# Optimization experiments

Hardware: AMD Instinct MI355X
Metric: run time of the kernel (lower is better)

Reference implementation:

```python
import jax, jax.numpy as jnp
import numpy as np

NUM_HEADS = 16
HEAD_DIM = 128
RMS_EPS = 1e-6


def _rms_norm(x):
    # RMSNorm over last dim, no learned weight
    return x * jax.lax.rsqrt(jnp.mean(jnp.square(x), axis=-1, keepdims=True) + RMS_EPS)


def _rotary_cos_sin(T, head_dim, dtype=jnp.float32):
    # half-truncated RoPE: quarter of dims get frequencies, next quarter gets freq 0
    dim_quarter = max(1, head_dim // 4)
    angular_freq = (1.0 / 1024.0) ** jnp.linspace(0.0, 1.0, dim_quarter, dtype=dtype)
    angular_freq = jnp.concatenate([angular_freq, jnp.zeros(dim_quarter, dtype=dtype)])  # [head_dim//2]
    t = jnp.arange(T, dtype=dtype)
    theta = t[:, None] * angular_freq[None, :]  # [T, head_dim//2]
    return jnp.cos(theta), jnp.sin(theta)


def _apply_rotary(x_BTHD, cos, sin):
    # x: [B,T,H,D]; cos/sin: [T, D//2]
    c = cos[None, :, None, :]
    s = sin[None, :, None, :]
    x1, x2 = jnp.split(x_BTHD, 2, axis=-1)
    y1 = x1 * c + x2 * s
    y2 = -x1 * s + x2 * c
    return jnp.concatenate([y1, y2], axis=-1)


def setup_inputs() -> dict:
    key = jax.random.key(0)
    k1, k2, k3 = jax.random.split(key, 3)
    B, T, dim = 1, 2048, 2048
    hdim = NUM_HEADS * HEAD_DIM
    std = 0.5 * dim ** (-0.5)
    x = jax.random.normal(k1, (B, T, dim), dtype=jnp.float32)
    Wqkv = jax.random.normal(k2, (3, hdim, dim), dtype=jnp.float32) * std
    Wout = jax.random.normal(k3, (dim, hdim), dtype=jnp.float32) * std
    return {"x": x, "Wqkv": Wqkv, "Wout": Wout}


def reference(x, Wqkv, Wout):
    B, T, dim = x.shape
    H, D = NUM_HEADS, HEAD_DIM
    scale = 1.0 / (D ** 0.5)

    # fused QKV projection: [B,T,3,H,D]
    qkv = jnp.einsum('btd,ehd->bteh'.replace('eh', 'f'), x, Wqkv.reshape(3 * H * D, dim))  # [B,T,3HD]
    qkv = qkv.reshape(B, T, 3, H, D)
    q, k, v = qkv[:, :, 0], qkv[:, :, 1], qkv[:, :, 2]  # each [B,T,H,D]

    q, k = _rms_norm(q), _rms_norm(k)
    cos, sin = _rotary_cos_sin(T, D, dtype=jnp.float32)
    q, k = _apply_rotary(q, cos, sin), _apply_rotary(k, cos, sin)

    # causal attention
    scores = jnp.einsum('bthd,bshd->bhts', q, k) * scale  # [B,H,T,T]
    causal = jnp.tril(jnp.ones((T, T), dtype=bool))
    scores = jnp.where(causal[None, None], scores, -jnp.inf)
    probs = jax.nn.softmax(scores, axis=-1)
    y = jnp.einsum('bhts,bshd->bthd', probs, v)  # [B,T,H,D]

    y = y.reshape(B, T, H * D)
    return y @ Wout.T
```

## Files before the change

### kernel.cpp

```cpp
#include <hip/hip_runtime.h>
#include <hip/hip_bf16.h>
#include <stdint.h>

typedef __hip_bfloat16 bf16;
typedef __bf16 bf16x8 __attribute__((ext_vector_type(8)));
typedef float f32x4 __attribute__((ext_vector_type(4)));

#define MFMA16(a, b, c) __builtin_amdgcn_mfma_f32_16x16x32_bf16((a), (b), (c), 0, 0, 0)

__device__ __forceinline__ void gload_lds16(const void* g, void* l) {
    __builtin_amdgcn_global_load_lds((const __attribute__((address_space(1))) void*)g,
                                     (__attribute__((address_space(3))) void*)l, 16, 0, 0);
}

struct alignas(16) B8 { bf16 v[8]; };
struct alignas(8)  B4 { bf16 v[4]; };

__global__ __launch_bounds__(256) void cast_all_k(
    const float* __restrict__ x, const float* __restrict__ wqkv, const float* __restrict__ wout,
    bf16* __restrict__ xb, bf16* __restrict__ wqkvb, bf16* __restrict__ woutb) {
    const size_t NX = (size_t)2048 * 2048 / 8;
    const size_t NW = (size_t)3 * 2048 * 2048 / 8;
    size_t i = (size_t)blockIdx.x * 256 + threadIdx.x;
    const float* s; bf16* d;
    if (i < NX)            { s = x;    d = xb; }
    else if (i < NX + NW)  { s = wqkv; d = wqkvb; i -= NX; }
    else                   { s = wout; d = woutb; i -= NX + NW; }
    float4 a = ((const float4*)s)[2 * i];
    float4 b = ((const float4*)s)[2 * i + 1];
    B8 t;
    t.v[0] = __float2bfloat16(a.x); t.v[1] = __float2bfloat16(a.y);
    t.v[2] = __float2bfloat16(a.z); t.v[3] = __float2bfloat16(a.w);
    t.v[4] = __float2bfloat16(b.x); t.v[5] = __float2bfloat16(b.y);
    t.v[6] = __float2bfloat16(b.z); t.v[7] = __float2bfloat16(b.w);
    ((B8*)d)[i] = t;
}

__global__ __launch_bounds__(256) void gemm_bt(
    const bf16* __restrict__ A, const bf16* __restrict__ B, float* __restrict__ C,
    int M, int N, int K) {
    __shared__ __align__(16) bf16 As[128 * 32];
    __shared__ __align__(16) bf16 Bs[128 * 32];
    const int t = threadIdx.x;
    const int lane = t & 63, w = t >> 6;
    const int wr = w >> 1, wc = w & 1;
    const int l15 = lane & 15, lg = lane >> 4;
    const int m0 = blockIdx.y * 128, n0 = blockIdx.x * 128;

    f32x4 acc[4][4] = {};

    for (int k0 = 0; k0 < K; k0 += 32) {
#pragma unroll
        for (int c = 0; c < 2; ++c) {
            int f = t + c * 256;
            int row = f >> 2, cb = f & 3;
            gload_lds16(&A[(size_t)(m0 + row) * K + k0 + cb * 8], &As[f * 8]);
            gload_lds16(&B[(size_t)(n0 + row) * K + k0 + cb * 8], &Bs[f * 8]);
        }
        __syncthreads();

        bf16x8 af[4], bfr[4];
#pragma unroll
        for (int mi = 0; mi < 4; ++mi)
            af[mi] = *(const bf16x8*)&As[(wr * 64 + mi * 16 + l15) * 32 + lg * 8];
#pragma unroll
        for (int ni = 0; ni < 4; ++ni)
            bfr[ni] = *(const bf16x8*)&Bs[(wc * 64 + ni * 16 + l15) * 32 + lg * 8];
#pragma unroll
        for (int mi = 0; mi < 4; ++mi)
#pragma unroll
            for (int ni = 0; ni < 4; ++ni)
                acc[mi][ni] = MFMA16(af[mi], bfr[ni], acc[mi][ni]);
        __syncthreads();
    }

#pragma unroll
    for (int mi = 0; mi < 4; ++mi) {
        int r0 = m0 + wr * 64 + mi * 16 + lg * 4;
#pragma unroll
        for (int ni = 0; ni < 4; ++ni) {
            int c0 = n0 + wc * 64 + ni * 16 + l15;
#pragma unroll
            for (int j = 0; j < 4; ++j)
                C[(size_t)(r0 + j) * N + c0] = acc[mi][ni][j];
        }
    }
}

__global__ __launch_bounds__(128) void normrope_k(
    const float* __restrict__ qkv, bf16* __restrict__ qb, bf16* __restrict__ kb) {
    const int t = blockIdx.x, h = blockIdx.y, d = threadIdx.x;
    const float* base = qkv + (size_t)t * 6144;
    float q = base[h * 128 + d];
    float k = base[2048 + h * 128 + d];

    __shared__ float red[4];
    __shared__ float qn[128], kn[128];
    float sq = q * q, sk = k * k;
#pragma unroll
    for (int m = 1; m <= 32; m <<= 1) {
        sq += __shfl_xor(sq, m);
        sk += __shfl_xor(sk, m);
    }
    if ((d & 63) == 0) { red[(d >> 6) * 2] = sq; red[(d >> 6) * 2 + 1] = sk; }
    __syncthreads();
    float rq = rsqrtf((red[0] + red[2]) * (1.0f / 128.0f) + 1e-6f);
    float rk = rsqrtf((red[1] + red[3]) * (1.0f / 128.0f) + 1e-6f);
    qn[d] = q * rq;
    kn[d] = k * rk;
    __syncthreads();

    int j = d & 63;
    float c = 1.0f, s = 0.0f;
    if (j < 32) {
        float af = exp2f(-10.0f * (float)j / 31.0f);
        float theta = (float)t * af;
        sincosf(theta, &s, &c);
    }
    float oq, ok;
    if (d < 64) { oq =  qn[d] * c + qn[d + 64] * s;  ok =  kn[d] * c + kn[d + 64] * s; }
    else        { oq = -qn[d - 64] * s + qn[d] * c;  ok = -kn[d - 64] * s + kn[d] * c; }

    size_t oidx = ((size_t)h * 2048 + t) * 128 + d;
    qb[oidx] = __float2bfloat16(oq * 0.08838834764831845f);
    kb[oidx] = __float2bfloat16(ok);
}

__global__ __launch_bounds__(256) void vtrans_k(
    const float* __restrict__ qkv, bf16* __restrict__ vt) {
    __shared__ bf16 Ts[64][72];
    const int t0 = blockIdx.x * 64, d0 = blockIdx.y * 64, h = blockIdx.z;
    const int tid = threadIdx.x;
#pragma unroll
    for (int it = 0; it < 4; ++it) {
        int f = tid + it * 256;
        int tl = f >> 4, dl = (f & 15) * 4;
        float4 v = *(const float4*)&qkv[(size_t)(t0 + tl) * 6144 + 4096 + h * 128 + d0 + dl];
        Ts[tl][dl + 0] = __float2bfloat16(v.x);
        Ts[tl][dl + 1] = __float2bfloat16(v.y);
        Ts[tl][dl + 2] = __float2bfloat16(v.z);
        Ts[tl][dl + 3] = __float2bfloat16(v.w);
    }
    __syncthreads();
#pragma unroll
    for (int it = 0; it < 2; ++it) {
        int f = tid + it * 256;
        int dl = f >> 3, tc = f & 7;
        B8 p;
#pragma unroll
        for (int i = 0; i < 8; ++i) p.v[i] = Ts[tc * 8 + i][dl];
        *(B8*)&vt[((size_t)h * 128 + d0 + dl) * 2048 + t0 + tc * 8] = p;
    }
}

__global__ __launch_bounds__(256) void attn_main_k(
    const bf16* __restrict__ qg, const bf16* __restrict__ kg,
    const bf16* __restrict__ vt, float* __restrict__ part) {
    const int T = 2048, D = 128;
    const int cz = blockIdx.x, qt = blockIdx.y, h = blockIdx.z;
    if (cz > (qt >> 3)) return;
    const int qb0 = qt * 64;
    const int kstart = cz * 512;
    const int kend = min(kstart + 512, (qt + 1) * 64);

    __shared__ __align__(16) bf16 Ks[64 * 128];
    __shared__ __align__(16) bf16 Vt[128 * 64];
    __shared__ __align__(16) bf16 Ps[4][16 * 64];

    const int t = threadIdx.x;
    const int lane = t & 63, w = t >> 6;
    const int l15 = lane & 15, lg = lane >> 4;

    const size_t qoff = ((size_t)h * T + qb0 + w * 16 + l15) * D;
    bf16x8 qf[4];
#pragma unroll
    for (int ks = 0; ks < 4; ++ks)
        qf[ks] = *(const bf16x8*)&qg[qoff + ks * 32 + lg * 8];

    f32x4 o[8] = {};
    float mrow[4] = {-1e30f, -1e30f, -1e30f, -1e30f};
    float lrow[4] = {0.f, 0.f, 0.f, 0.f};

    for (int k0 = kstart; k0 < kend; k0 += 64) {
#pragma unroll
        for (int c = 0; c < 4; ++c) {
            int f = t + c * 256;
            int krow = f >> 4, kc = f & 15;
            gload_lds16(&kg[((size_t)h * T + k0 + krow) * D + ((kc ^ (krow & 15)) * 8)],
                        &Ks[f * 8]);
            int dr = f >> 3, vc = f & 7;
            gload_lds16(&vt[((size_t)h * D + dr) * T + k0 + ((vc ^ (dr & 7)) * 8)],
                        &Vt[f * 8]);
        }
        __syncthreads();

        f32x4 sc[4] = {};
#pragma unroll
        for (int ks = 0; ks < 4; ++ks) {
#pragma unroll
            for (int nb = 0; nb < 4; ++nb) {
                int key = nb * 16 + l15;
                int c = ks * 4 + lg;
                bf16x8 kf = *(const bf16x8*)&Ks[key * 128 + ((c ^ (key & 15)) * 8)];
                sc[nb] = MFMA16(qf[ks], kf, sc[nb]);
            }
        }

        const bool diag = (k0 == qb0);
        const int qrow_base = qb0 + w * 16 + lg * 4;
#pragma unroll
        for (int j = 0; j < 4; ++j) {
            float s0 = sc[0][j], s1 = sc[1][j], s2 = sc[2][j], s3 = sc[3][j];
            if (diag) {
                int qrow = qrow_base + j;
                if (k0 + l15 > qrow)      s0 = -1e30f;
                if (k0 + 16 + l15 > qrow) s1 = -1e30f;
                if (k0 + 32 + l15 > qrow) s2 = -1e30f;
                if (k0 + 48 + l15 > qrow) s3 = -1e30f;
            }
            float tm = fmaxf(fmaxf(s0, s1), fmaxf(s2, s3));
            tm = fmaxf(tm, __shfl_xor(tm, 1));
            tm = fmaxf(tm, __shfl_xor(tm, 2));
            tm = fmaxf(tm, __shfl_xor(tm, 4));
            tm = fmaxf(tm, __shfl_xor(tm, 8));
            float mnew = fmaxf(mrow[j], tm);
            float fac = __expf(mrow[j] - mnew);
            float p0 = __expf(s0 - mnew), p1 = __expf(s1 - mnew);
            float p2 = __expf(s2 - mnew), p3 = __expf(s3 - mnew);
            float ps = (p0 + p1) + (p2 + p3);
            ps += __shfl_xor(ps, 1);
            ps += __shfl_xor(ps, 2);
            ps += __shfl_xor(ps, 4);
            ps += __shfl_xor(ps, 8);
            lrow[j] = lrow[j] * fac + ps;
            mrow[j] = mnew;
#pragma unroll
            for (int nd = 0; nd < 8; ++nd) o[nd][j] *= fac;
            int prow = lg * 4 + j;
            int sub = l15 & 7, hi = l15 >> 3;
            bf16* pw = &Ps[w][prow * 64 + sub];
            pw[(((0 + hi) ^ (prow & 7)) * 8)] = __float2bfloat16(p0);
            pw[(((2 + hi) ^ (prow & 7)) * 8)] = __float2bfloat16(p1);
            pw[(((4 + hi) ^ (prow & 7)) * 8)] = __float2bfloat16(p2);
            pw[(((6 + hi) ^ (prow & 7)) * 8)] = __float2bfloat16(p3);
        }

#pragma unroll
        for (int hk = 0; hk < 2; ++hk) {
            bf16x8 pf = *(const bf16x8*)&Ps[w][l15 * 64 + (((hk * 4 + lg) ^ (l15 & 7)) * 8)];
#pragma unroll
            for (int nd = 0; nd < 8; ++nd) {
                int dd = nd * 16 + l15;
                bf16x8 vf = *(const bf16x8*)&Vt[dd * 64 + (((hk * 4 + lg) ^ (dd & 7)) * 8)];
                o[nd] = MFMA16(pf, vf, o[nd]);
            }
        }
        __syncthreads();
    }

    int b = qt >> 3, rr = qt & 7;
    int slot = h * 80 + qt + 4 * b * (b - 1) + rr * b + cz;
    float* rec = part + (size_t)slot * 8320;
    if (l15 == 0) {
#pragma unroll
        for (int j = 0; j < 4; ++j) {
            rec[w * 16 + lg * 4 + j] = mrow[j];
            rec[64 + w * 16 + lg * 4 + j] = lrow[j];
        }
    }
#pragma unroll
    for (int nd = 0; nd < 8; ++nd)
#pragma unroll
        for (int j = 0; j < 4; ++j)
            rec[128 + (w * 16 + lg * 4 + j) * 128 + nd * 16 + l15] = o[nd][j];
}

__global__ __launch_bounds__(256) void attn_merge_k(
    const float* __restrict__ part, bf16* __restrict__ y) {
    const int qt = blockIdx.x, h = blockIdx.y, tid = threadIdx.x;
    const int nch = (qt >> 3) + 1;
    int b = qt >> 3, rr = qt & 7;
    const int base = h * 80 + qt + 4 * b * (b - 1) + rr * b;
    const int r = tid >> 2;
    const int d0 = (tid & 3) * 32;

    float mi[4], li[4], wgt[4];
    float M = -1e30f;
#pragma unroll
    for (int i = 0; i < 4; ++i) {
        if (i < nch) {
            mi[i] = part[(size_t)(base + i) * 8320 + r];
            li[i] = part[(size_t)(base + i) * 8320 + 64 + r];
            M = fmaxf(M, mi[i]);
        } else { mi[i] = -1e30f; li[i] = 0.f; }
    }
    float L = 0.f;
#pragma unroll
    for (int i = 0; i < 4; ++i) {
        wgt[i] = (i < nch) ? __expf(mi[i] - M) : 0.f;
        L += li[i] * wgt[i];
    }
    float invL = 1.0f / L;

    bf16* yrow = &y[(size_t)(qt * 64 + r) * 2048 + h * 128 + d0];
#pragma unroll
    for (int dd = 0; dd < 32; dd += 4) {
        float a0 = 0.f, a1 = 0.f, a2 = 0.f, a3 = 0.f;
#pragma unroll
        for (int i = 0; i < 4; ++i) {
            if (i < nch) {
                const float4 ov = *(const float4*)&part[(size_t)(base + i) * 8320 + 128 + r * 128 + d0 + dd];
                a0 += wgt[i] * ov.x; a1 += wgt[i] * ov.y;
                a2 += wgt[i] * ov.z; a3 += wgt[i] * ov.w;
            }
        }
        B4 p;
        p.v[0] = __float2bfloat16(a0 * invL);
        p.v[1] = __float2bfloat16(a1 * invL);
        p.v[2] = __float2bfloat16(a2 * invL);
        p.v[3] = __float2bfloat16(a3 * invL);
        *(B4*)&yrow[dd] = p;
    }
}

extern "C" void kernel_launch(void* const* d_in, const int* in_sizes, int n_in,
                              void* d_out, int out_size, void* d_ws, size_t ws_size,
                              hipStream_t stream) {
    const float* x    = (const float*)d_in[0];
    const float* wqkv = (const float*)d_in[1];
    const float* wout = (const float*)d_in[2];
    float* out = (float*)d_out;

    char* ws = (char*)d_ws;
    bf16*  xb    = (bf16*)(ws);
    bf16*  wqkvb = (bf16*)(ws + 8388608);
    bf16*  woutb = (bf16*)(ws + 33554432);
    float* qkvf  = (float*)(ws + 41943040);
    bf16*  qb    = (bf16*)(ws + 92274688);
    bf16*  kb    = (bf16*)(ws + 100663296);
    bf16*  vt    = (bf16*)(ws + 109051904);
    bf16*  yb    = (bf16*)(ws + 117440512);

    cast_all_k<<<10240, 256, 0, stream>>>(x, wqkv, wout, xb, wqkvb, woutb);
    gemm_bt<<<dim3(48, 16), 256, 0, stream>>>(xb, wqkvb, qkvf, 2048, 6144, 2048);
    normrope_k<<<dim3(2048, 16), 128, 0, stream>>>(qkvf, qb, kb);
    vtrans_k<<<dim3(32, 2, 16), 256, 0, stream>>>(qkvf, vt);
    attn_main_k<<<dim3(4, 32, 16), 256, 0, stream>>>(qb, kb, vt, qkvf);
    attn_merge_k<<<dim3(32, 16), 256, 0, stream>>>(qkvf, yb);
    gemm_bt<<<dim3(16, 16), 256, 0, stream>>>(yb, woutb, out, 2048, 2048, 2048);
}
```

Measured before the change: 388.3 us.

## Double-buffer LDS tiles in GEMM and attention kernels to overlap loads

Both the projection GEMM and the attention main loop now keep two LDS buffers and issue the global-to-LDS loads for the next K/V or A/B tile before computing on the current one. Partial vmcnt waits replace the full __syncthreads drain, so memory latency can overlap with MFMA work. This doubles LDS use (the attention kernel grows to roughly 80KB), which can reduce occupancy. It also relies on hand-placed s_waitcnt/s_barrier ordering being correct.

```diff
diff --git a/kernel.cpp b/kernel.cpp
--- a/kernel.cpp
+++ b/kernel.cpp
@@ -39,40 +39,60 @@
 __global__ __launch_bounds__(256) void gemm_bt(
     const bf16* __restrict__ A, const bf16* __restrict__ B, float* __restrict__ C,
     int M, int N, int K) {
-    __shared__ __align__(16) bf16 As[128 * 32];
-    __shared__ __align__(16) bf16 Bs[128 * 32];
+    __shared__ __align__(16) bf16 As[2][128 * 32];
+    __shared__ __align__(16) bf16 Bs[2][128 * 32];
     const int t = threadIdx.x;
     const int lane = t & 63, w = t >> 6;
     const int wr = w >> 1, wc = w & 1;
     const int l15 = lane & 15, lg = lane >> 4;
     const int m0 = blockIdx.y * 128, n0 = blockIdx.x * 128;
 
+    const int row = t >> 2, cb = t & 3;
+    const int row1 = (t + 256) >> 2, cb1 = t & 3;
+
     f32x4 acc[4][4] = {};
 
+#define G_STAGE(buf, k0)                                                        \
+    do {                                                                        \
+        gload_lds16(&A[(size_t)(m0 + row) * K + (k0) + cb * 8],                 \
+                    &As[buf][t * 8]);                                           \
+        gload_lds16(&B[(size_t)(n0 + row) * K + (k0) + cb * 8],                 \
+                    &Bs[buf][t * 8]);                                           \
+        gload_lds16(&A[(size_t)(m0 + row1) * K + (k0) + cb1 * 8],               \
+                    &As[buf][(t + 256) * 8]);                                   \
+        gload_lds16(&B[(size_t)(n0 + row1) * K + (k0) + cb1 * 8],               \
+                    &Bs[buf][(t + 256) * 8]);                                   \
+    } while (0)
+
+    G_STAGE(0, 0);
+    int cur = 0;
     for (int k0 = 0; k0 < K; k0 += 32) {
-#pragma unroll
-        for (int c = 0; c < 2; ++c) {
-            int f = t + c * 256;
-            int row = f >> 2, cb = f & 3;
-            gload_lds16(&A[(size_t)(m0 + row) * K + k0 + cb * 8], &As[f * 8]);
-            gload_lds16(&B[(size_t)(n0 + row) * K + k0 + cb * 8], &Bs[f * 8]);
-        }
-        __syncthreads();
+        const bool hn = (k0 + 32 < K);
+        if (hn) {
+            G_STAGE(cur ^ 1, k0 + 32);
+            asm volatile("s_waitcnt vmcnt(4)" ::: "memory");
+        } else {
+            asm volatile("s_waitcnt vmcnt(0)" ::: "memory");
+        }
+        __builtin_amdgcn_s_barrier();
+        __builtin_amdgcn_sched_barrier(0);
 
         bf16x8 af[4], bfr[4];
 #pragma unroll
         for (int mi = 0; mi < 4; ++mi)
-            af[mi] = *(const bf16x8*)&As[(wr * 64 + mi * 16 + l15) * 32 + lg * 8];
+            af[mi] = *(const bf16x8*)&As[cur][(wr * 64 + mi * 16 + l15) * 32 + lg * 8];
 #pragma unroll
         for (int ni = 0; ni < 4; ++ni)
-            bfr[ni] = *(const bf16x8*)&Bs[(wc * 64 + ni * 16 + l15) * 32 + lg * 8];
+            bfr[ni] = *(const bf16x8*)&Bs[cur][(wc * 64 + ni * 16 + l15) * 32 + lg * 8];
 #pragma unroll
         for (int mi = 0; mi < 4; ++mi)
 #pragma unroll
             for (int ni = 0; ni < 4; ++ni)
                 acc[mi][ni] = MFMA16(af[mi], bfr[ni], acc[mi][ni]);
-        __syncthreads();
-    }
+        __builtin_amdgcn_s_barrier();
+        cur ^= 1;
+    }
+#undef G_STAGE
 
 #pragma unroll
     for (int mi = 0; mi < 4; ++mi) {
@@ -163,8 +183,8 @@
     const int kstart = cz * 512;
     const int kend = min(kstart + 512, (qt + 1) * 64);
 
-    __shared__ __align__(16) bf16 Ks[64 * 128];
-    __shared__ __align__(16) bf16 Vt[128 * 64];
+    __shared__ __align__(16) bf16 Ks[2][64 * 128];
+    __shared__ __align__(16) bf16 Vs[2][64 * 128];
     __shared__ __align__(16) bf16 Ps[4][16 * 64];
 
     const int t = threadIdx.x;
@@ -181,18 +201,32 @@
     float mrow[4] = {-1e30f, -1e30f, -1e30f, -1e30f};
     float lrow[4] = {0.f, 0.f, 0.f, 0.f};
 
+#define A_STAGE(buf, k0)                                                         \
+    do {                                                                         \
+        _Pragma("unroll")                                                        \
+        for (int c = 0; c < 4; ++c) {                                            \
+            int f = t + c * 256;                                                 \
+            int krow = f >> 4, kc = f & 15;                                      \
+            gload_lds16(&kg[((size_t)h * T + (k0) + krow) * D + ((kc ^ (krow & 15)) * 8)], \
+                        &Ks[buf][f * 8]);                                        \
+            int dr = f >> 3, vc = f & 7;                                         \
+            gload_lds16(&vt[((size_t)h * D + dr) * T + (k0) + ((vc ^ (dr & 7)) * 8)],      \
+                        &Vs[buf][f * 8]);                                        \
+        }                                                                        \
+    } while (0)
+
+    A_STAGE(0, kstart);
+    int cur = 0;
     for (int k0 = kstart; k0 < kend; k0 += 64) {
-#pragma unroll
-        for (int c = 0; c < 4; ++c) {
-            int f = t + c * 256;
-            int krow = f >> 4, kc = f & 15;
-            gload_lds16(&kg[((size_t)h * T + k0 + krow) * D + ((kc ^ (krow & 15)) * 8)],
-                        &Ks[f * 8]);
-            int dr = f >> 3, vc = f & 7;
-            gload_lds16(&vt[((size_t)h * D + dr) * T + k0 + ((vc ^ (dr & 7)) * 8)],
-                        &Vt[f * 8]);
-        }
-        __syncthreads();
+        const bool hn = (k0 + 64 < kend);
+        if (hn) {
+            A_STAGE(cur ^ 1, k0 + 64);
+            asm volatile("s_waitcnt vmcnt(8)" ::: "memory");
+        } else {
+            asm volatile("s_waitcnt vmcnt(0)" ::: "memory");
+        }
+        __builtin_amdgcn_s_barrier();
+        __builtin_amdgcn_sched_barrier(0);
 
         f32x4 sc[4] = {};
 #pragma unroll
@@ -201,7 +235,7 @@
             for (int nb = 0; nb < 4; ++nb) {
                 int key = nb * 16 + l15;
                 int c = ks * 4 + lg;
-                bf16x8 kf = *(const bf16x8*)&Ks[key * 128 + ((c ^ (key & 15)) * 8)];
+                bf16x8 kf = *(const bf16x8*)&Ks[cur][key * 128 + ((c ^ (key & 15)) * 8)];
                 sc[nb] = MFMA16(qf[ks], kf, sc[nb]);
             }
         }
@@ -251,12 +285,14 @@
 #pragma unroll
             for (int nd = 0; nd < 8; ++nd) {
                 int dd = nd * 16 + l15;
-                bf16x8 vf = *(const bf16x8*)&Vt[dd * 64 + (((hk * 4 + lg) ^ (dd & 7)) * 8)];
+                bf16x8 vf = *(const bf16x8*)&Vs[cur][dd * 64 + (((hk * 4 + lg) ^ (dd & 7)) * 8)];
                 o[nd] = MFMA16(pf, vf, o[nd]);
             }
         }
-        __syncthreads();
-    }
+        __builtin_amdgcn_s_barrier();
+        cur ^= 1;
+    }
+#undef A_STAGE
 
     int b = qt >> 3, rr = qt & 7;
     int slot = h * 80 + qt + 4 * b * (b - 1) + rr * b + cz;
```

After: 371.8 us. 1.04x faster.
